# Kernel optimization log

Hardware: AMD Instinct MI355X
Metric: run time of the kernel (lower is better)

Reference implementation:

```python
import jax, jax.numpy as jnp
import numpy as np

B, T, S = 128, 256, 64
IN, H, K, CSL, OUT = 3, 512, 10, 60, 121


def setup_inputs() -> dict:
    key = jax.random.key(0)
    ks = jax.random.split(key, 10)
    s = lambda k, shape, sc: jax.random.normal(k, shape, jnp.float32) * sc
    return {
        "x": jax.random.normal(ks[0], (B, T, IN), jnp.float32),
        "sentences": jax.random.uniform(ks[1], (B, S, CSL), dtype=jnp.float32),
        "h1_h": jnp.zeros((B, H), jnp.float32),
        "h1_c": jnp.zeros((B, H), jnp.float32),
        "h2_h": jnp.zeros((B, H), jnp.float32),
        "h2_c": jnp.zeros((B, H), jnp.float32),
        # LSTMCell params (torch gate order i,f,g,o); b = b_ih + b_hh fused
        "W_ih_cell": s(ks[2], (4 * H, IN + CSL), 0.04),
        "W_hh_cell": s(ks[3], (4 * H, H), 0.04),
        "b_cell": jnp.zeros((4 * H,), jnp.float32),
        # second-layer nn.LSTM params
        "W_ih_l": s(ks[4], (4 * H, IN + CSL + H), 0.04),
        "W_hh_l": s(ks[5], (4 * H, H), 0.04),
        "b_l": jnp.zeros((4 * H,), jnp.float32),
        # fc1 -> window params, fc2 -> output
        "W1": s(ks[6], (3 * K, H), 0.04),
        "b1": jnp.zeros((3 * K,), jnp.float32),
        "W2": s(ks[7], (OUT, H), 0.04),
        "b2": jnp.zeros((OUT,), jnp.float32),
    }


def _lstm_step(h, c, xt, W_ih, W_hh, b):
    g = xt @ W_ih.T + h @ W_hh.T + b
    i, f, gg, o = jnp.split(g, 4, axis=-1)
    c2 = jax.nn.sigmoid(f) * c + jax.nn.sigmoid(i) * jnp.tanh(gg)
    h2 = jax.nn.sigmoid(o) * jnp.tanh(c2)
    return h2, c2


def reference(x, sentences, h1_h, h1_c, h2_h, h2_c,
              W_ih_cell, W_hh_cell, b_cell,
              W_ih_l, W_hh_l, b_l, W1, b1, W2, b2):
    u = jnp.arange(1, S + 1, dtype=x.dtype)[:, None]  # [S,1] char positions

    def step1(carry, xt):
        h, c, p = carry
        ip = jnp.exp(h @ W1.T + b1)                                     # [B,3K]
        # kappa part subtracts the previous step's kappa (quirk of the source)
        p_new = jnp.concatenate([ip[:, :2 * K], ip[:, 2 * K:] - p[:, 2 * K:]], axis=-1)
        a, be, ka = jnp.split(p_new[:, None, :], 3, axis=-1)            # each [B,1,K]
        phi = (a * jnp.exp(-be * (ka - u) ** 2)).sum(-1)                # [B,S]
        win = jnp.einsum('bs,bsc->bc', phi, sentences)                  # [B,CSL]
        h2, c2 = _lstm_step(h, c, jnp.concatenate([xt, win], axis=-1),
                            W_ih_cell, W_hh_cell, b_cell)
        return (h2, c2, p_new), (h2, win)

    xs = jnp.swapaxes(x, 0, 1)                                          # [T,B,IN]
    p0 = jnp.zeros((x.shape[0], 3 * K), x.dtype)
    (h1f, c1f, _), (hx, wins) = jax.lax.scan(step1, (h1_h, h1_c, p0), xs)

    feat = jnp.concatenate([xs, wins, hx], axis=-1)                     # [T,B,IN+CSL+H]

    def step2(carry, xt):
        h, c = carry
        h2, c2 = _lstm_step(h, c, xt, W_ih_l, W_hh_l, b_l)
        return (h2, c2), h2

    (h2f, c2f), ys = jax.lax.scan(step2, (h2_h, h2_c), feat)
    y = jnp.swapaxes(ys, 0, 1).reshape(-1, H)                           # [B*T,H]
    out = y @ W2.T + b2                                                 # [B*T,OUT]
    return out, h1f, c1f, h2f, c2f
```

## Files before the change

kernel.cpp:

```cpp
#include <hip/hip_runtime.h>
#include <hip/hip_bf16.h>
#include <math.h>

typedef __attribute__((ext_vector_type(8))) short short8;
typedef __attribute__((ext_vector_type(4))) float floatx4;

#define DEVFN static __device__ __forceinline__

constexpr int B = 128, T = 256, H = 512;
constexpr int OUTW = 121;
constexpr int SLOTW = 1664;
constexpr int LOOF  = 1088;
constexpr int SLOTE = B * SLOTW;
constexpr int NSLOT = T + 2;
constexpr int NG  = 2048;
constexpr int K1  = 576,  K1C = 18;
constexpr int K2  = 1088, K2C = 34;
constexpr int KW1P = 584, KW2P = 1096;

constexpr int O_WH1 = 0;
constexpr int O_WL1 = 37376;
constexpr int O_W1S = 74752;
constexpr int O_GSM = 137152;
constexpr int O_HS  = 145472;
constexpr int O_PP  = 147584;
constexpr int O_IPL = 148544;
constexpr int O_KL  = 148664;
constexpr int O_PHL = 148704;
constexpr int O_WAC = 148960;
constexpr int O_KPR = 149920;
constexpr int O_B1S = 149960;
constexpr int O_BIA = 150080;
constexpr int O_WH2 = 0;
constexpr int O_WL2 = 70144;
constexpr int O_GS2 = 140288;
constexpr int O_BI2 = 148608;
constexpr int LDS_SZ = 150272;

DEVFN __hip_bfloat16 bhi(float v) { return __float2bfloat16(v); }
DEVFN __hip_bfloat16 blo(float v, __hip_bfloat16 h) { return __float2bfloat16(v - __bfloat162float(h)); }
DEVFN float bf2f(__hip_bfloat16 h) { return __bfloat162float(h); }
DEVFN unsigned short bbits(__hip_bfloat16 h) { union { __hip_bfloat16 h; unsigned short u; } c; c.h = h; return c.u; }
DEVFN unsigned int pack2(float a, float b) {
  return (unsigned int)bbits(bhi(a)) | ((unsigned int)bbits(bhi(b)) << 16);
}
DEVFN void ast(unsigned int* p, unsigned int v) {
  __hip_atomic_store(p, v, __ATOMIC_RELAXED, __HIP_MEMORY_SCOPE_AGENT);
}
DEVFN int ald(int* p) {
  return __hip_atomic_load(p, __ATOMIC_RELAXED, __HIP_MEMORY_SCOPE_AGENT);
}

DEVFN void waitflags(int* flags, int n, int target) {
  if ((int)threadIdx.x < n) {
    int g = 0;
    while (ald(&flags[threadIdx.x]) < target && g < (1 << 22)) { ++g; __builtin_amdgcn_s_sleep(1); }
  }
  __syncthreads();
}
DEVFN void dualwait(int* fa, int* fb, int target) {
  int tid = threadIdx.x;
  if (tid < 128) {
    int* f = (tid < 64) ? fa + tid : fb + (tid - 64);
    int g = 0;
    while (ald(f) < target && g < (1 << 22)) { ++g; __builtin_amdgcn_s_sleep(1); }
  }
  __syncthreads();
}
DEVFN void flag_store(int* flag, int val) {
  asm volatile("s_waitcnt vmcnt(0)" ::: "memory");
  __syncthreads();
  if (threadIdx.x == 0)
    __hip_atomic_store(flag, val, __ATOMIC_RELAXED, __HIP_MEMORY_SCOPE_AGENT);
}

__global__ __launch_bounds__(256) void k_pre(
    const float* __restrict__ x, const float* __restrict__ h1h, const float* __restrict__ h2h,
    const float* __restrict__ Wihc, const float* __restrict__ Whhc, const float* __restrict__ bc,
    const float* __restrict__ Wihl, const float* __restrict__ Whhl, const float* __restrict__ bl,
    const float* __restrict__ W2,
    __hip_bfloat16* __restrict__ fxHL,
    __hip_bfloat16* __restrict__ wc1, __hip_bfloat16* __restrict__ wc1l,
    __hip_bfloat16* __restrict__ wc2, __hip_bfloat16* __restrict__ wc2l,
    __hip_bfloat16* __restrict__ w2b, float* __restrict__ bi1, float* __restrict__ bi2,
    int* __restrict__ ctl)
{
  int idx = blockIdx.x * 256 + threadIdx.x;
  const int nwc1 = NG * K1, nwc2 = NG * K2, nw2b = 128 * 512, nbi = 2 * NG;
  const int nfh = B * H, nxj = T * B, nctl = 512;
  if (idx < nwc1) {
    int n = idx / K1, col = idx - n * K1;
    int src = (n & 3) * H + (n >> 2);
    float v = (col < 63) ? Wihc[src * 63 + col]
            : (col == 63 ? 0.f : Whhc[src * 512 + (col - 64)]);
    __hip_bfloat16 h = bhi(v);
    wc1[n * K1 + col] = h; wc1l[n * K1 + col] = blo(v, h);
    return;
  }
  idx -= nwc1;
  if (idx < nwc2) {
    int n = idx / K2, col = idx - n * K2;
    int src = (n & 3) * H + (n >> 2);
    float v;
    if (col < 63)       v = Wihl[src * 575 + col];
    else if (col == 63) v = 0.f;
    else if (col < 576) v = Wihl[src * 575 + (col - 1)];
    else                v = Whhl[src * 512 + (col - 576)];
    __hip_bfloat16 h = bhi(v);
    wc2[n * K2 + col] = h; wc2l[n * K2 + col] = blo(v, h);
    return;
  }
  idx -= nwc2;
  if (idx < nw2b) {
    int n = idx >> 9, col = idx & 511;
    w2b[idx] = bhi(n < OUTW ? W2[n * 512 + col] : 0.f);
    return;
  }
  idx -= nw2b;
  if (idx < nbi) {
    int n = idx & (NG - 1);
    int src = (n & 3) * H + (n >> 2);
    if (idx < NG) bi1[n] = bc[src]; else bi2[n] = bl[src];
    return;
  }
  idx -= nbi;
  if (idx < nfh) {
    int b = idx >> 9, j = idx & 511;
    float v = h1h[idx];
    __hip_bfloat16 h = bhi(v);
    fxHL[b * SLOTW + 64 + j] = h;
    fxHL[b * SLOTW + LOOF + 64 + j] = blo(v, h);
    return;
  }
  idx -= nfh;
  if (idx < nfh) {
    int b = idx >> 9, j = idx & 511;
    fxHL[(size_t)SLOTE + b * SLOTW + 576 + j] = bhi(h2h[idx]);
    return;
  }
  idx -= nfh;
  if (idx < nxj) {
    int t = idx >> 7, b = idx & 127;
    float x0 = x[(b * T + t) * 3 + 0], x1 = x[(b * T + t) * 3 + 1];
    unsigned int* ph = (unsigned int*)(fxHL + (size_t)(t + 1) * SLOTE + b * SLOTW);
    ph[0] = pack2(x0, x1);
    unsigned int* pl = (unsigned int*)(fxHL + (size_t)(t + 1) * SLOTE + b * SLOTW + LOOF);
    pl[0] = 0u;
    return;
  }
  idx -= nxj;
  if (idx < nctl) ctl[idx] = 0;
}

template <int KWP>
DEVFN void gemm3(int tid, const __hip_bfloat16* __restrict__ Aslot, int m0,
                 const __hip_bfloat16* __restrict__ Wh, const __hip_bfloat16* __restrict__ Wl,
                 int cbeg, int cend, floatx4& a0, floatx4& a1)
{
  const int lane = tid & 63, wv = tid >> 6;
  const int lm = lane & 15, lk = (lane >> 4) << 3;
  const __hip_bfloat16* Ar = Aslot + (size_t)(m0 + wv * 16 + lm) * SLOTW;
  const __hip_bfloat16* W0h = Wh + lm * KWP;
  const __hip_bfloat16* W1h = Wh + (16 + lm) * KWP;
  const __hip_bfloat16* W0l = Wl + lm * KWP;
  const __hip_bfloat16* W1l = Wl + (16 + lm) * KWP;
  #pragma unroll 4
  for (int c = cbeg; c < cend; ++c) {
    int col = c * 32 + lk;
    short8 va  = *(const short8*)(Ar + col);
    short8 ua  = *(const short8*)(Ar + LOOF + col);
    short8 vb0 = *(const short8*)(W0h + col);
    short8 vb1 = *(const short8*)(W1h + col);
    short8 ub0 = *(const short8*)(W0l + col);
    short8 ub1 = *(const short8*)(W1l + col);
    a0 = __builtin_amdgcn_mfma_f32_16x16x32_bf16(va, vb0, a0, 0, 0, 0);
    a1 = __builtin_amdgcn_mfma_f32_16x16x32_bf16(va, vb1, a1, 0, 0, 0);
    a0 = __builtin_amdgcn_mfma_f32_16x16x32_bf16(va, ub0, a0, 0, 0, 0);
    a1 = __builtin_amdgcn_mfma_f32_16x16x32_bf16(va, ub1, a1, 0, 0, 0);
    a0 = __builtin_amdgcn_mfma_f32_16x16x32_bf16(ua, vb0, a0, 0, 0, 0);
    a1 = __builtin_amdgcn_mfma_f32_16x16x32_bf16(ua, vb1, a1, 0, 0, 0);
  }
}

template <int KWP>
DEVFN void gemm2(int tid, const __hip_bfloat16* __restrict__ Aslot, int m0,
                 const __hip_bfloat16* __restrict__ Wh, const __hip_bfloat16* __restrict__ Wl,
                 int cbeg, int cend, floatx4& a0, floatx4& a1)
{
  const int lane = tid & 63, wv = tid >> 6;
  const int lm = lane & 15, lk = (lane >> 4) << 3;
  const __hip_bfloat16* Ar = Aslot + (size_t)(m0 + wv * 16 + lm) * SLOTW;
  const __hip_bfloat16* W0h = Wh + lm * KWP;
  const __hip_bfloat16* W1h = Wh + (16 + lm) * KWP;
  const __hip_bfloat16* W0l = Wl + lm * KWP;
  const __hip_bfloat16* W1l = Wl + (16 + lm) * KWP;
  #pragma unroll 4
  for (int c = cbeg; c < cend; ++c) {
    int col = c * 32 + lk;
    short8 va  = *(const short8*)(Ar + col);
    short8 vb0 = *(const short8*)(W0h + col);
    short8 vb1 = *(const short8*)(W1h + col);
    short8 ub0 = *(const short8*)(W0l + col);
    short8 ub1 = *(const short8*)(W1l + col);
    a0 = __builtin_amdgcn_mfma_f32_16x16x32_bf16(va, vb0, a0, 0, 0, 0);
    a1 = __builtin_amdgcn_mfma_f32_16x16x32_bf16(va, vb1, a1, 0, 0, 0);
    a0 = __builtin_amdgcn_mfma_f32_16x16x32_bf16(va, ub0, a0, 0, 0, 0);
    a1 = __builtin_amdgcn_mfma_f32_16x16x32_bf16(va, ub1, a1, 0, 0, 0);
  }
}

DEVFN void store_gsm(int tid, float* Gsm, floatx4 a0, floatx4 a1) {
  const int lane = tid & 63, wv = tid >> 6;
  const int lm = lane & 15, rr = (lane >> 4) << 2;
  #pragma unroll
  for (int r = 0; r < 4; ++r) {
    Gsm[lm * 65 + wv * 16 + rr + r]        = a0[r];
    Gsm[(16 + lm) * 65 + wv * 16 + rr + r] = a1[r];
  }
}

__global__ __launch_bounds__(256, 1) void k_persist(
    __hip_bfloat16* __restrict__ fxHL,
    const __hip_bfloat16* __restrict__ wc1, const __hip_bfloat16* __restrict__ wc1l,
    const __hip_bfloat16* __restrict__ wc2, const __hip_bfloat16* __restrict__ wc2l,
    const float* __restrict__ bi1, const float* __restrict__ bi2,
    const float* __restrict__ c1init, const float* __restrict__ c2init,
    const float* __restrict__ xin, const float* __restrict__ sent,
    const float* __restrict__ W1, const float* __restrict__ b1,
    int* __restrict__ ctl,
    float* __restrict__ h1f, float* __restrict__ c1f,
    float* __restrict__ h2f, float* __restrict__ c2f)
{
  extern __shared__ char sm[];
  const int gid = blockIdx.x, tid = threadIdx.x;

  if (gid < 128) {
    const int nt1 = gid >> 1, mh = gid & 1;
    const int n0 = nt1 * 32, m0 = mh * 64;
    const int brow = mh * 64 + nt1;
    int* wf = ctl + mh * 64;
    int* hf = ctl + 128 + mh * 64;
    __hip_bfloat16* smWh = (__hip_bfloat16*)(sm + O_WH1);
    __hip_bfloat16* smWl = (__hip_bfloat16*)(sm + O_WL1);
    float* smW1 = (float*)(sm + O_W1S);
    float* Gsm  = (float*)(sm + O_GSM);
    float* hs   = (float*)(sm + O_HS);
    float* winv = (float*)(sm + O_HS);
    float* pp   = (float*)(sm + O_PP);
    float* ipl  = (float*)(sm + O_IPL);
    float* kl   = (float*)(sm + O_KL);
    float* phl  = (float*)(sm + O_PHL);
    float* wac  = (float*)(sm + O_WAC);
    float* kpr  = (float*)(sm + O_KPR);
    float* b1s  = (float*)(sm + O_B1S);
    float* bia  = (float*)(sm + O_BIA);

    for (int i = tid; i < 32 * 72; i += 256) {
      int r = i / 72, c8 = (i - r * 72) * 8;
      *(short8*)(smWh + r * KW1P + c8) = *(const short8*)(wc1  + (size_t)(n0 + r) * K1 + c8);
      *(short8*)(smWl + r * KW1P + c8) = *(const short8*)(wc1l + (size_t)(n0 + r) * K1 + c8);
    }
    for (int i = tid; i < 30 * 512; i += 256) {
      int j = i >> 9, c = i & 511;
      smW1[j * 520 + (c >> 6) * 65 + (c & 63)] = W1[i];
    }
    if (tid < 30) b1s[tid] = b1[tid];
    if (tid < 10) kpr[tid] = 0.f;
    if (tid < 32) bia[tid] = bi1[n0 + tid];
    __syncthreads();

    float creg[2];
    {
      int ml = tid >> 2, ppi = tid & 3;
      creg[0] = c1init[(m0 + ml) * H + nt1 * 8 + 2 * ppi + 0];
      creg[1] = c1init[(m0 + ml) * H + nt1 * 8 + 2 * ppi + 1];
    }

    for (int t = 0; t < T; ++t) {
      __hip_bfloat16* S1 = fxHL + (size_t)(t + 1) * SLOTE;
      __hip_bfloat16* S0 = fxHL + (size_t)t * SLOTE;

      waitflags(hf, 64, t);

      for (int i = tid; i < 512; i += 256) {
        float hv = bf2f(S0[brow * SLOTW + 64 + i]) + bf2f(S0[brow * SLOTW + LOOF + 64 + i]);
        hs[(i >> 6) * 66 + (i & 63)] = hv;
      }
      __syncthreads();
      if (tid < 240) {
        int j = tid >> 3, p = tid & 7;
        const float* wp = smW1 + j * 520 + p * 65;
        const float* hv = hs + p * 66;
        float s = 0.f;
        #pragma unroll 8
        for (int k = 0; k < 64; ++k) s += hv[k] * wp[k];
        pp[tid] = s;
      }
      __syncthreads();
      if (tid < 30) {
        float s = b1s[tid];
        #pragma unroll
        for (int p = 0; p < 8; ++p) s += pp[tid * 8 + p];
        ipl[tid] = expf(s);
      }
      __syncthreads();
      if (tid < 10) {
        float kap = ipl[20 + tid] - kpr[tid];
        kpr[tid] = kap; kl[tid] = kap;
      }
      __syncthreads();
      if (tid < 64) {
        float u = (float)(tid + 1);
        float acc = 0.f;
        #pragma unroll
        for (int k = 0; k < 10; ++k) {
          float d = kl[k] - u;
          acc += ipl[k] * expf(-ipl[10 + k] * d * d);
        }
        phl[tid] = acc;
      }
      __syncthreads();
      if (tid < 240) {
        int c = tid >> 2, p = tid & 3;
        float acc = 0.f;
        #pragma unroll
        for (int s0 = 0; s0 < 16; ++s0)
          acc += phl[p * 16 + s0] * sent[(brow * 64 + p * 16 + s0) * 60 + c];
        wac[tid] = acc;
      }
      __syncthreads();
      if (tid < 60)
        winv[tid] = wac[tid * 4] + wac[tid * 4 + 1] + wac[tid * 4 + 2] + wac[tid * 4 + 3];
      __syncthreads();
      if (tid < 31) {
        int d = 1 + tid;
        int c0 = 2 * d, c1 = 2 * d + 1;
        float v0 = (c0 == 2) ? xin[(brow * T + t) * 3 + 2] : winv[c0 - 3];
        float v1 = (c1 == 63) ? 0.f : winv[c1 - 3];
        __hip_bfloat16 h0 = bhi(v0), h1v = bhi(v1);
        unsigned int* prow = (unsigned int*)(S1 + brow * SLOTW);
        ast(prow + d, (unsigned int)bbits(h0) | ((unsigned int)bbits(h1v) << 16));
        ast(prow + (LOOF >> 1) + d,
            (unsigned int)bbits(blo(v0, h0)) | ((unsigned int)bbits(blo(v1, h1v)) << 16));
      }
      flag_store(wf + nt1, t + 1);

      floatx4 a0 = {0.f, 0.f, 0.f, 0.f}, a1 = a0;
      gemm3<KW1P>(tid, S0, m0, smWh, smWl, 2, K1C, a0, a1);
      waitflags(wf, 64, t + 1);
      gemm3<KW1P>(tid, S1, m0, smWh, smWl, 0, 2, a0, a1);
      store_gsm(tid, Gsm, a0, a1);
      __syncthreads();

      {
        int ml = tid >> 2, ppi = tid & 3;
        float v[2];
        #pragma unroll
        for (int j = 0; j < 2; ++j) {
          int nl = ppi * 8 + j * 4;
          float gi = Gsm[(nl + 0) * 65 + ml] + bia[nl + 0];
          float gf = Gsm[(nl + 1) * 65 + ml] + bia[nl + 1];
          float gg = Gsm[(nl + 2) * 65 + ml] + bia[nl + 2];
          float go = Gsm[(nl + 3) * 65 + ml] + bia[nl + 3];
          float ig = 1.f / (1.f + expf(-gi));
          float fg = 1.f / (1.f + expf(-gf));
          float gt = tanhf(gg);
          float og = 1.f / (1.f + expf(-go));
          float cn = fg * creg[j] + ig * gt;
          v[j] = og * tanhf(cn);
          creg[j] = cn;
        }
        __hip_bfloat16 h0 = bhi(v[0]), h1v = bhi(v[1]);
        unsigned int* prow = (unsigned int*)(S1 + (m0 + ml) * SLOTW);
        int dw = 32 + nt1 * 4 + ppi;
        ast(prow + dw, (unsigned int)bbits(h0) | ((unsigned int)bbits(h1v) << 16));
        ast(prow + (LOOF >> 1) + dw,
            (unsigned int)bbits(blo(v[0], h0)) | ((unsigned int)bbits(blo(v[1], h1v)) << 16));
        if (t == T - 1) {
          int hg = nt1 * 8 + 2 * ppi;
          h1f[(m0 + ml) * H + hg]     = v[0];  c1f[(m0 + ml) * H + hg]     = creg[0];
          h1f[(m0 + ml) * H + hg + 1] = v[1];  c1f[(m0 + ml) * H + hg + 1] = creg[1];
        }
      }
      flag_store(hf + nt1, t + 1);
    }
  } else {
    const int g = gid - 128;
    const int nt2 = g >> 1, mh = g & 1;
    const int n0 = nt2 * 32, m0 = mh * 64;
    int* wf  = ctl + mh * 64;
    int* hf  = ctl + 128 + mh * 64;
    int* h2g = ctl + 256 + mh * 64;
    __hip_bfloat16* smWh = (__hip_bfloat16*)(sm + O_WH2);
    __hip_bfloat16* smWl = (__hip_bfloat16*)(sm + O_WL2);
    float* Gsm = (float*)(sm + O_GS2);
    float* bia = (float*)(sm + O_BI2);

    for (int i = tid; i < 32 * 136; i += 256) {
      int r = i / 136, c8 = (i - r * 136) * 8;
      *(short8*)(smWh + r * KW2P + c8) = *(const short8*)(wc2  + (size_t)(n0 + r) * K2 + c8);
      *(short8*)(smWl + r * KW2P + c8) = *(const short8*)(wc2l + (size_t)(n0 + r) * K2 + c8);
    }
    if (tid < 32) bia[tid] = bi2[n0 + tid];
    __syncthreads();

    float creg[2];
    {
      int ml = tid >> 2, ppi = tid & 3;
      creg[0] = c2init[(m0 + ml) * H + nt2 * 8 + 2 * ppi + 0];
      creg[1] = c2init[(m0 + ml) * H + nt2 * 8 + 2 * ppi + 1];
    }

    for (int t = 0; t < T; ++t) {
      __hip_bfloat16* S1 = fxHL + (size_t)(t + 1) * SLOTE;
      __hip_bfloat16* S2 = fxHL + (size_t)(t + 2) * SLOTE;

      waitflags(h2g, 64, t);
      floatx4 a0 = {0.f, 0.f, 0.f, 0.f}, a1 = a0;
      gemm2<KW2P>(tid, S1, m0, smWh, smWl, K1C, K2C, a0, a1);
      dualwait(hf, wf, t + 1);
      gemm3<KW2P>(tid, S1, m0, smWh, smWl, 0, K1C, a0, a1);
      store_gsm(tid, Gsm, a0, a1);
      __syncthreads();

      {
        int ml = tid >> 2, ppi = tid & 3;
        float v[2];
        #pragma unroll
        for (int j = 0; j < 2; ++j) {
          int nl = ppi * 8 + j * 4;
          float gi = Gsm[(nl + 0) * 65 + ml] + bia[nl + 0];
          float gf = Gsm[(nl + 1) * 65 + ml] + bia[nl + 1];
          float gg = Gsm[(nl + 2) * 65 + ml] + bia[nl + 2];
          float go = Gsm[(nl + 3) * 65 + ml] + bia[nl + 3];
          float ig = 1.f / (1.f + expf(-gi));
          float fg = 1.f / (1.f + expf(-gf));
          float gt = tanhf(gg);
          float og = 1.f / (1.f + expf(-go));
          float cn = fg * creg[j] + ig * gt;
          v[j] = og * tanhf(cn);
          creg[j] = cn;
        }
        __hip_bfloat16 h0 = bhi(v[0]), h1v = bhi(v[1]);
        unsigned int* prow = (unsigned int*)(S2 + (m0 + ml) * SLOTW);
        int dw = 288 + nt2 * 4 + ppi;
        ast(prow + dw, (unsigned int)bbits(h0) | ((unsigned int)bbits(h1v) << 16));
        if (t == T - 1) {
          int hg = nt2 * 8 + 2 * ppi;
          h2f[(m0 + ml) * H + hg]     = v[0];  c2f[(m0 + ml) * H + hg]     = creg[0];
          h2f[(m0 + ml) * H + hg + 1] = v[1];  c2f[(m0 + ml) * H + hg + 1] = creg[1];
        }
      }
      flag_store(h2g + nt2, t + 1);
    }
  }
}

__global__ __launch_bounds__(256) void k_out(
    const __hip_bfloat16* __restrict__ fxHL, const __hip_bfloat16* __restrict__ w2b,
    const float* __restrict__ b2, float* __restrict__ dout)
{
  int bid = blockIdx.x, tid = threadIdx.x;
  int mblk = bid >> 1, nblk = bid & 1;
  int wv = tid >> 6, lane = tid & 63;
  int lm = lane & 15, lk = (lane >> 4) << 3;
  int m0 = mblk * 128 + wv * 32;
  int n0 = nblk * 64;
  int r0 = m0 + lm, r1 = m0 + 16 + lm;
  const __hip_bfloat16* a0p = fxHL + (size_t)((r0 & 255) + 2) * SLOTE + (r0 >> 8) * SLOTW + 576;
  const __hip_bfloat16* a1p = fxHL + (size_t)((r1 & 255) + 2) * SLOTE + (r1 >> 8) * SLOTW + 576;
  floatx4 zz = {0.f, 0.f, 0.f, 0.f};
  floatx4 acc[2][4];
  #pragma unroll
  for (int mt = 0; mt < 2; ++mt)
    #pragma unroll
    for (int nt = 0; nt < 4; ++nt) acc[mt][nt] = zz;
  #pragma unroll
  for (int c = 0; c < 16; ++c) {
    int col = c * 32 + lk;
    short8 va0 = *(const short8*)(a0p + col);
    short8 va1 = *(const short8*)(a1p + col);
    short8 vb[4];
    #pragma unroll
    for (int nt = 0; nt < 4; ++nt)
      vb[nt] = *(const short8*)(w2b + (size_t)(n0 + nt * 16 + lm) * 512 + col);
    #pragma unroll
    for (int nt = 0; nt < 4; ++nt) {
      acc[0][nt] = __builtin_amdgcn_mfma_f32_16x16x32_bf16(va0, vb[nt], acc[0][nt], 0, 0, 0);
      acc[1][nt] = __builtin_amdgcn_mfma_f32_16x16x32_bf16(va1, vb[nt], acc[1][nt], 0, 0, 0);
    }
  }
  int rr = (lane >> 4) << 2;
  #pragma unroll
  for (int mt = 0; mt < 2; ++mt)
    #pragma unroll
    for (int nt = 0; nt < 4; ++nt)
      #pragma unroll
      for (int r = 0; r < 4; ++r) {
        int m = m0 + mt * 16 + rr + r;
        int n = n0 + nt * 16 + lm;
        if (n < OUTW) dout[(size_t)m * OUTW + n] = acc[mt][nt][r] + b2[n];
      }
}

extern "C" void kernel_launch(void* const* d_in, const int* in_sizes, int n_in,
                              void* d_out, int out_size, void* d_ws, size_t ws_size,
                              hipStream_t stream)
{
  (void)in_sizes; (void)n_in; (void)out_size; (void)ws_size;
  const float* x    = (const float*)d_in[0];
  const float* sent = (const float*)d_in[1];
  const float* h1h  = (const float*)d_in[2];
  const float* h1c  = (const float*)d_in[3];
  const float* h2h  = (const float*)d_in[4];
  const float* h2c  = (const float*)d_in[5];
  const float* Wihc = (const float*)d_in[6];
  const float* Whhc = (const float*)d_in[7];
  const float* bc   = (const float*)d_in[8];
  const float* Wihl = (const float*)d_in[9];
  const float* Whhl = (const float*)d_in[10];
  const float* bl   = (const float*)d_in[11];
  const float* W1   = (const float*)d_in[12];
  const float* b1   = (const float*)d_in[13];
  const float* W2   = (const float*)d_in[14];
  const float* b2   = (const float*)d_in[15];

  float* out = (float*)d_out;
  float* h1f = out + (size_t)B * T * OUTW;
  float* c1f = h1f + (size_t)B * H;
  float* h2f = c1f + (size_t)B * H;
  float* c2f = h2f + (size_t)B * H;

  char* p = (char*)d_ws;
  auto carve = [&](size_t bytes) { char* r = p; p += (bytes + 255) & ~(size_t)255; return r; };
  __hip_bfloat16* fxHL = (__hip_bfloat16*)carve((size_t)NSLOT * SLOTE * 2);
  __hip_bfloat16* wc1  = (__hip_bfloat16*)carve((size_t)NG * K1 * 2);
  __hip_bfloat16* wc1l = (__hip_bfloat16*)carve((size_t)NG * K1 * 2);
  __hip_bfloat16* wc2  = (__hip_bfloat16*)carve((size_t)NG * K2 * 2);
  __hip_bfloat16* wc2l = (__hip_bfloat16*)carve((size_t)NG * K2 * 2);
  __hip_bfloat16* w2b  = (__hip_bfloat16*)carve((size_t)128 * 512 * 2);
  float* bi1 = (float*)carve((size_t)NG * 4);
  float* bi2 = (float*)carve((size_t)NG * 4);
  int*   ctl = (int*)carve((size_t)512 * 4);

  static bool attr_set = false;
  if (!attr_set) {
    (void)hipFuncSetAttribute((const void*)k_persist,
                              hipFuncAttributeMaxDynamicSharedMemorySize, LDS_SZ);
    attr_set = true;
  }

  k_pre<<<14226, 256, 0, stream>>>(x, h1h, h2h, Wihc, Whhc, bc, Wihl, Whhl, bl, W2,
                                   fxHL, wc1, wc1l, wc2, wc2l, w2b, bi1, bi2, ctl);
  k_persist<<<256, 256, LDS_SZ, stream>>>(fxHL, wc1, wc1l, wc2, wc2l, bi1, bi2,
                                          h1c, h2c, x, sent, W1, b1, ctl,
                                          h1f, c1f, h2f, c2f);
  k_out<<<512, 256, 0, stream>>>(fxHL, w2b, b2, out);
}
```

Measured before the change: 3.328 ms.

## Prefetch recurrent GEMM operands into registers and cache sentences in LDS

In both persistent recurrence branches, the activation fragments for the MFMA GEMMs are now loaded from global memory into register arrays right after each flag wait, in one batch. The generic gemm loops are replaced with fully unrolled ones that consume these prefetched registers. This is meant to hide global load latency on the serial per-timestep critical path. Layer 1 also copies its sentence block into LDS once and reads the x input early. The cost is more LDS and much higher register pressure, which could cause spills.

After: 3.005 ms. 1.11x faster.

```diff
diff --git a/kernel.cpp b/kernel.cpp
--- a/kernel.cpp
+++ b/kernel.cpp
@@ -22,20 +22,21 @@
 constexpr int O_WL1 = 37376;
 constexpr int O_W1S = 74752;
 constexpr int O_GSM = 137152;
-constexpr int O_HS  = 145472;
-constexpr int O_PP  = 147584;
-constexpr int O_IPL = 148544;
-constexpr int O_KL  = 148664;
-constexpr int O_PHL = 148704;
-constexpr int O_WAC = 148960;
-constexpr int O_KPR = 149920;
-constexpr int O_B1S = 149960;
-constexpr int O_BIA = 150080;
+constexpr int O_HS  = 137152;
+constexpr int O_PP  = 139264;
+constexpr int O_IPL = 145472;
+constexpr int O_KL  = 145592;
+constexpr int O_PHL = 145632;
+constexpr int O_WAC = 145888;
+constexpr int O_KPR = 146848;
+constexpr int O_B1S = 146888;
+constexpr int O_BIA = 147008;
+constexpr int O_SENT = 147136;
 constexpr int O_WH2 = 0;
 constexpr int O_WL2 = 70144;
 constexpr int O_GS2 = 140288;
 constexpr int O_BI2 = 148608;
-constexpr int LDS_SZ = 150272;
+constexpr int LDS_SZ = 162496;
 
 DEVFN __hip_bfloat16 bhi(float v) { return __float2bfloat16(v); }
 DEVFN __hip_bfloat16 blo(float v, __hip_bfloat16 h) { return __float2bfloat16(v - __bfloat162float(h)); }
@@ -56,6 +57,7 @@
     int g = 0;
     while (ald(&flags[threadIdx.x]) < target && g < (1 << 22)) { ++g; __builtin_amdgcn_s_sleep(1); }
   }
+  asm volatile("" ::: "memory");
   __syncthreads();
 }
 DEVFN void dualwait(int* fa, int* fb, int target) {
@@ -65,6 +67,7 @@
     int g = 0;
     while (ald(f) < target && g < (1 << 22)) { ++g; __builtin_amdgcn_s_sleep(1); }
   }
+  asm volatile("" ::: "memory");
   __syncthreads();
 }
 DEVFN void flag_store(int* flag, int val) {
@@ -182,33 +185,6 @@
   }
 }
 
-template <int KWP>
-DEVFN void gemm2(int tid, const __hip_bfloat16* __restrict__ Aslot, int m0,
-                 const __hip_bfloat16* __restrict__ Wh, const __hip_bfloat16* __restrict__ Wl,
-                 int cbeg, int cend, floatx4& a0, floatx4& a1)
-{
-  const int lane = tid & 63, wv = tid >> 6;
-  const int lm = lane & 15, lk = (lane >> 4) << 3;
-  const __hip_bfloat16* Ar = Aslot + (size_t)(m0 + wv * 16 + lm) * SLOTW;
-  const __hip_bfloat16* W0h = Wh + lm * KWP;
-  const __hip_bfloat16* W1h = Wh + (16 + lm) * KWP;
-  const __hip_bfloat16* W0l = Wl + lm * KWP;
-  const __hip_bfloat16* W1l = Wl + (16 + lm) * KWP;
-  #pragma unroll 4
-  for (int c = cbeg; c < cend; ++c) {
-    int col = c * 32 + lk;
-    short8 va  = *(const short8*)(Ar + col);
-    short8 vb0 = *(const short8*)(W0h + col);
-    short8 vb1 = *(const short8*)(W1h + col);
-    short8 ub0 = *(const short8*)(W0l + col);
-    short8 ub1 = *(const short8*)(W1l + col);
-    a0 = __builtin_amdgcn_mfma_f32_16x16x32_bf16(va, vb0, a0, 0, 0, 0);
-    a1 = __builtin_amdgcn_mfma_f32_16x16x32_bf16(va, vb1, a1, 0, 0, 0);
-    a0 = __builtin_amdgcn_mfma_f32_16x16x32_bf16(va, ub0, a0, 0, 0, 0);
-    a1 = __builtin_amdgcn_mfma_f32_16x16x32_bf16(va, ub1, a1, 0, 0, 0);
-  }
-}
-
 DEVFN void store_gsm(int tid, float* Gsm, floatx4 a0, floatx4 a1) {
   const int lane = tid & 63, wv = tid >> 6;
   const int lm = lane & 15, rr = (lane >> 4) << 2;
@@ -233,6 +209,8 @@
 {
   extern __shared__ char sm[];
   const int gid = blockIdx.x, tid = threadIdx.x;
+  const int lane = tid & 63, wv = tid >> 6;
+  const int lm = lane & 15, lk = (lane >> 4) << 3;
 
   if (gid < 128) {
     const int nt1 = gid >> 1, mh = gid & 1;
@@ -254,6 +232,7 @@
     float* kpr  = (float*)(sm + O_KPR);
     float* b1s  = (float*)(sm + O_B1S);
     float* bia  = (float*)(sm + O_BIA);
+    float* ssent = (float*)(sm + O_SENT);
 
     for (int i = tid; i < 32 * 72; i += 256) {
       int r = i / 72, c8 = (i - r * 72) * 8;
@@ -264,6 +243,8 @@
       int j = i >> 9, c = i & 511;
       smW1[j * 520 + (c >> 6) * 65 + (c & 63)] = W1[i];
     }
+    for (int i = tid; i < 64 * 60; i += 256)
+      ssent[i] = sent[(size_t)brow * 64 * 60 + i];
     if (tid < 30) b1s[tid] = b1[tid];
     if (tid < 10) kpr[tid] = 0.f;
     if (tid < 32) bia[tid] = bi1[n0 + tid];
@@ -276,17 +257,34 @@
       creg[1] = c1init[(m0 + ml) * H + nt1 * 8 + 2 * ppi + 1];
     }
 
+    const __hip_bfloat16* W0h = smWh + lm * KW1P;
+    const __hip_bfloat16* W1h = smWh + (16 + lm) * KW1P;
+    const __hip_bfloat16* W0l = smWl + lm * KW1P;
+    const __hip_bfloat16* W1l = smWl + (16 + lm) * KW1P;
+
     for (int t = 0; t < T; ++t) {
       __hip_bfloat16* S1 = fxHL + (size_t)(t + 1) * SLOTE;
       __hip_bfloat16* S0 = fxHL + (size_t)t * SLOTE;
 
       waitflags(hf, 64, t);
 
-      for (int i = tid; i < 512; i += 256) {
-        float hv = bf2f(S0[brow * SLOTW + 64 + i]) + bf2f(S0[brow * SLOTW + LOOF + 64 + i]);
-        hs[(i >> 6) * 66 + (i & 63)] = hv;
-      }
-      __syncthreads();
+      const __hip_bfloat16* wrow = S0 + (size_t)brow * SLOTW;
+      __hip_bfloat16 a0h = wrow[64 + tid];
+      __hip_bfloat16 a0l = wrow[LOOF + 64 + tid];
+      __hip_bfloat16 a1h = wrow[64 + 256 + tid];
+      __hip_bfloat16 a1l = wrow[LOOF + 64 + 256 + tid];
+      float x2v = xin[(brow * T + t) * 3 + 2];
+      const __hip_bfloat16* Ar = S0 + (size_t)(m0 + wv * 16 + lm) * SLOTW;
+      short8 pva[16], pua[16];
+      #pragma unroll
+      for (int c = 0; c < 16; ++c) {
+        pva[c] = *(const short8*)(Ar + (c + 2) * 32 + lk);
+        pua[c] = *(const short8*)(Ar + LOOF + (c + 2) * 32 + lk);
+      }
+      hs[(tid >> 6) * 66 + (tid & 63)] = bf2f(a0h) + bf2f(a0l);
+      hs[((tid + 256) >> 6) * 66 + (tid & 63)] = bf2f(a1h) + bf2f(a1l);
+      __syncthreads();
+
       if (tid < 240) {
         int j = tid >> 3, p = tid & 7;
         const float* wp = smW1 + j * 520 + p * 65;
@@ -325,7 +323,7 @@
         float acc = 0.f;
         #pragma unroll
         for (int s0 = 0; s0 < 16; ++s0)
-          acc += phl[p * 16 + s0] * sent[(brow * 64 + p * 16 + s0) * 60 + c];
+          acc += phl[p * 16 + s0] * ssent[(p * 16 + s0) * 60 + c];
         wac[tid] = acc;
       }
       __syncthreads();
@@ -335,10 +333,10 @@
       if (tid < 31) {
         int d = 1 + tid;
         int c0 = 2 * d, c1 = 2 * d + 1;
-        float v0 = (c0 == 2) ? xin[(brow * T + t) * 3 + 2] : winv[c0 - 3];
+        float v0 = (c0 == 2) ? x2v : winv[c0 - 3];
         float v1 = (c1 == 63) ? 0.f : winv[c1 - 3];
         __hip_bfloat16 h0 = bhi(v0), h1v = bhi(v1);
-        unsigned int* prow = (unsigned int*)(S1 + brow * SLOTW);
+        unsigned int* prow = (unsigned int*)(S1 + (size_t)brow * SLOTW);
         ast(prow + d, (unsigned int)bbits(h0) | ((unsigned int)bbits(h1v) << 16));
         ast(prow + (LOOF >> 1) + d,
             (unsigned int)bbits(blo(v0, h0)) | ((unsigned int)bbits(blo(v1, h1v)) << 16));
@@ -346,7 +344,20 @@
       flag_store(wf + nt1, t + 1);
 
       floatx4 a0 = {0.f, 0.f, 0.f, 0.f}, a1 = a0;
-      gemm3<KW1P>(tid, S0, m0, smWh, smWl, 2, K1C, a0, a1);
+      #pragma unroll
+      for (int c = 0; c < 16; ++c) {
+        int col = (c + 2) * 32 + lk;
+        short8 vb0 = *(const short8*)(W0h + col);
+        short8 vb1 = *(const short8*)(W1h + col);
+        short8 ub0 = *(const short8*)(W0l + col);
+        short8 ub1 = *(const short8*)(W1l + col);
+        a0 = __builtin_amdgcn_mfma_f32_16x16x32_bf16(pva[c], vb0, a0, 0, 0, 0);
+        a1 = __builtin_amdgcn_mfma_f32_16x16x32_bf16(pva[c], vb1, a1, 0, 0, 0);
+        a0 = __builtin_amdgcn_mfma_f32_16x16x32_bf16(pva[c], ub0, a0, 0, 0, 0);
+        a1 = __builtin_amdgcn_mfma_f32_16x16x32_bf16(pva[c], ub1, a1, 0, 0, 0);
+        a0 = __builtin_amdgcn_mfma_f32_16x16x32_bf16(pua[c], vb0, a0, 0, 0, 0);
+        a1 = __builtin_amdgcn_mfma_f32_16x16x32_bf16(pua[c], vb1, a1, 0, 0, 0);
+      }
       waitflags(wf, 64, t + 1);
       gemm3<KW1P>(tid, S1, m0, smWh, smWl, 0, 2, a0, a1);
       store_gsm(tid, Gsm, a0, a1);
@@ -371,7 +382,7 @@
           creg[j] = cn;
         }
         __hip_bfloat16 h0 = bhi(v[0]), h1v = bhi(v[1]);
-        unsigned int* prow = (unsigned int*)(S1 + (m0 + ml) * SLOTW);
+        unsigned int* prow = (unsigned int*)(S1 + (size_t)(m0 + ml) * SLOTW);
         int dw = 32 + nt1 * 4 + ppi;
         ast(prow + dw, (unsigned int)bbits(h0) | ((unsigned int)bbits(h1v) << 16));
         ast(prow + (LOOF >> 1) + dw,
@@ -411,15 +422,55 @@
       creg[1] = c2init[(m0 + ml) * H + nt2 * 8 + 2 * ppi + 1];
     }
 
+    const __hip_bfloat16* W0h = smWh + lm * KW2P;
+    const __hip_bfloat16* W1h = smWh + (16 + lm) * KW2P;
+    const __hip_bfloat16* W0l = smWl + lm * KW2P;
+    const __hip_bfloat16* W1l = smWl + (16 + lm) * KW2P;
+
     for (int t = 0; t < T; ++t) {
       __hip_bfloat16* S1 = fxHL + (size_t)(t + 1) * SLOTE;
       __hip_bfloat16* S2 = fxHL + (size_t)(t + 2) * SLOTE;
+      const __hip_bfloat16* Ar = S1 + (size_t)(m0 + wv * 16 + lm) * SLOTW;
 
       waitflags(h2g, 64, t);
+      short8 pv2[16];
+      #pragma unroll
+      for (int c = 0; c < 16; ++c)
+        pv2[c] = *(const short8*)(Ar + (K1C + c) * 32 + lk);
       floatx4 a0 = {0.f, 0.f, 0.f, 0.f}, a1 = a0;
-      gemm2<KW2P>(tid, S1, m0, smWh, smWl, K1C, K2C, a0, a1);
+      #pragma unroll
+      for (int c = 0; c < 16; ++c) {
+        int col = (K1C + c) * 32 + lk;
+        short8 vb0 = *(const short8*)(W0h + col);
+        short8 vb1 = *(const short8*)(W1h + col);
+        short8 ub0 = *(const short8*)(W0l + col);
+        short8 ub1 = *(const short8*)(W1l + col);
+        a0 = __builtin_amdgcn_mfma_f32_16x16x32_bf16(pv2[c], vb0, a0, 0, 0, 0);
+        a1 = __builtin_amdgcn_mfma_f32_16x16x32_bf16(pv2[c], vb1, a1, 0, 0, 0);
+        a0 = __builtin_amdgcn_mfma_f32_16x16x32_bf16(pv2[c], ub0, a0, 0, 0, 0);
+        a1 = __builtin_amdgcn_mfma_f32_16x16x32_bf16(pv2[c], ub1, a1, 0, 0, 0);
+      }
       dualwait(hf, wf, t + 1);
-      gemm3<KW2P>(tid, S1, m0, smWh, smWl, 0, K1C, a0, a1);
+      short8 qv[18], qu[18];
+      #pragma unroll
+      for (int c = 0; c < 18; ++c) {
+        qv[c] = *(const short8*)(Ar + c * 32 + lk);
+        qu[c] = *(const short8*)(Ar + LOOF + c * 32 + lk);
+      }
+      #pragma unroll
+      for (int c = 0; c < 18; ++c) {
+        int col = c * 32 + lk;
+        short8 vb0 = *(const short8*)(W0h + col);
+        short8 vb1 = *(const short8*)(W1h + col);
+        short8 ub0 = *(const short8*)(W0l + col);
+        short8 ub1 = *(const short8*)(W1l + col);
+        a0 = __builtin_amdgcn_mfma_f32_16x16x32_bf16(qv[c], vb0, a0, 0, 0, 0);
+        a1 = __builtin_amdgcn_mfma_f32_16x16x32_bf16(qv[c], vb1, a1, 0, 0, 0);
+        a0 = __builtin_amdgcn_mfma_f32_16x16x32_bf16(qv[c], ub0, a0, 0, 0, 0);
+        a1 = __builtin_amdgcn_mfma_f32_16x16x32_bf16(qv[c], ub1, a1, 0, 0, 0);
+        a0 = __builtin_amdgcn_mfma_f32_16x16x32_bf16(qu[c], vb0, a0, 0, 0, 0);
+        a1 = __builtin_amdgcn_mfma_f32_16x16x32_bf16(qu[c], vb1, a1, 0, 0, 0);
+      }
       store_gsm(tid, Gsm, a0, a1);
       __syncthreads();
 
@@ -442,7 +493,7 @@
           creg[j] = cn;
         }
         __hip_bfloat16 h0 = bhi(v[0]), h1v = bhi(v[1]);
-        unsigned int* prow = (unsigned int*)(S2 + (m0 + ml) * SLOTW);
+        unsigned int* prow = (unsigned int*)(S2 + (size_t)(m0 + ml) * SLOTW);
         int dw = 288 + nt2 * 4 + ppi;
         ast(prow + dw, (unsigned int)bbits(h0) | ((unsigned int)bbits(h1v) << 16));
         if (t == T - 1) {
```
